# Kernel tuning notes

Measured on AMD Instinct MI355X. Metric: run time of the kernel, lower is better.

Reference implementation:

```python
import jax, jax.numpy as jnp
import numpy as np

H = 16   # nheads
WIN = 64 # window_size (= sqrt(n) so the b,h,n//w,n//w,dk view is valid)


def setup_inputs() -> dict:
    key = jax.random.key(0)
    ks = jax.random.split(key, 7)
    b, n, d = 4, 4096, 1024
    q = jax.random.normal(ks[0], (b, n, d), dtype=jnp.float32)
    k = jax.random.normal(ks[1], (b, n, d), dtype=jnp.float32)
    v = jax.random.normal(ks[2], (b, n, d), dtype=jnp.float32)
    # nn.Linear(d, d, bias=False) weights, stored torch-style as (out, in)
    Wq = jax.random.normal(ks[3], (d, d), dtype=jnp.float32) * 0.02
    Wk = jax.random.normal(ks[4], (d, d), dtype=jnp.float32) * 0.02
    Wv = jax.random.normal(ks[5], (d, d), dtype=jnp.float32) * 0.02
    Wo = jax.random.normal(ks[6], (d, d), dtype=jnp.float32) * 0.02
    return {"q": q, "k": k, "v": v, "Wq": Wq, "Wk": Wk, "Wv": Wv, "Wo": Wo, "window": 1}


def _attention(q, k, v, Wq, Wk, Wv, Wo, window):
    b, qn, d = q.shape
    n = k.shape[1]
    dk = d // H
    # torch Linear: x @ W.T
    qh = (q @ Wq.T).reshape(b, qn, H, dk).transpose(0, 2, 1, 3)  # (b,h,qn,dk)
    kh = (k @ Wk.T).reshape(b, n, H, dk).transpose(0, 2, 1, 3)
    vh = (v @ Wv.T).reshape(b, n, H, dk).transpose(0, 2, 1, 3)
    if window and WIN > 0:
        nw = n // WIN  # requires n == nw*nw, as in the torch .view
        qh = qh.reshape(b, H, nw, nw, dk)
        kh = kh.reshape(b, H, nw, nw, dk)
        vh = vh.reshape(b, H, nw, nw, dk)
    scale = jnp.float32(1.0) / jnp.sqrt(jnp.float32(dk))
    attn = jnp.einsum('...qd,...kd->...qk', qh, kh) * scale  # block-local scores
    attn = jax.nn.softmax(attn, axis=-1)
    o = jnp.einsum('...qk,...kd->...qd', attn, vh)
    # torch: attn.transpose(1, -2).contiguous().view(b, qn, d)
    o = jnp.swapaxes(o, 1, -2).reshape(b, qn, d)
    return o @ Wo.T


def reference(q, k, v, Wq, Wk, Wv, Wo, window):
    return _attention(q, k, v, Wq, Wk, Wv, Wo, window)
```

## Files before the change

kernel.cpp:

```cpp
#include <hip/hip_runtime.h>


typedef unsigned short u16;
typedef unsigned int u32;
typedef __bf16 bf16x8 __attribute__((ext_vector_type(8)));
typedef float f32x4 __attribute__((ext_vector_type(4)));
typedef u16 u16x8 __attribute__((ext_vector_type(8)));

__device__ __forceinline__ u16 f2bf(float f) {
  u32 u = __builtin_bit_cast(u32, f);
  u += 0x7fffu + ((u >> 16) & 1u);
  return (u16)(u >> 16);
}

__device__ __forceinline__ void cvt8_store(const float* __restrict__ src,
                                           u16* __restrict__ dst, size_t i) {
  const float4 a = *(const float4*)(src + i);
  const float4 b = *(const float4*)(src + i + 4);
  u16x8 r;
  r[0] = f2bf(a.x); r[1] = f2bf(a.y); r[2] = f2bf(a.z); r[3] = f2bf(a.w);
  r[4] = f2bf(b.x); r[5] = f2bf(b.y); r[6] = f2bf(b.z); r[7] = f2bf(b.w);
  *(u16x8*)(dst + i) = r;
}

__global__ __launch_bounds__(256) void cvt_kernel(const float* __restrict__ src,
                                                  u16* __restrict__ dst) {
  cvt8_store(src, dst, ((size_t)blockIdx.x * 256 + threadIdx.x) * 8);
}

__global__ __launch_bounds__(256) void cvtw_kernel(
    const float* __restrict__ Wq, const float* __restrict__ Wk,
    const float* __restrict__ Wv, const float* __restrict__ Wo,
    u16* __restrict__ dst) {
  const float* src = (blockIdx.z == 0) ? Wq : (blockIdx.z == 1) ? Wk
                   : (blockIdx.z == 2) ? Wv : Wo;
  cvt8_store(src, dst + (size_t)blockIdx.z * 1048576,
             ((size_t)blockIdx.x * 256 + threadIdx.x) * 8);
}

__device__ __forceinline__ void cp16(const u16* g, u16* l) {
  __builtin_amdgcn_global_load_lds((const __attribute__((address_space(1))) void*)g,
                                   (__attribute__((address_space(3))) void*)l, 16, 0, 0);
}

__global__ __launch_bounds__(256, 2) void gemm_bt_kernel(
    const u16* __restrict__ A, const u16* __restrict__ B, void* __restrict__ Cv,
    int cf) {
  constexpr int N = 1024, K = 1024;
  __shared__ u16 lA[128 * 32];
  __shared__ u16 lB[128 * 32];
  const int tid = threadIdx.x;
  const int lane = tid & 63, w = tid >> 6;
  const int quad = lane >> 4, lr = lane & 15;
  const int lid = blockIdx.x;
  const int xcd = lid & 7, slot = lid >> 3;
  const int m0 = (xcd * 16 + (slot >> 3)) * 128;
  const int n0 = (slot & 7) * 128;
  const int wr = (w >> 1) * 64, wc = (w & 1) * 64;

  const int ch1 = tid, ch2 = tid + 256;
  const u16* Ag1 = A + (size_t)(m0 + (ch1 >> 2)) * K + (ch1 & 3) * 8;
  const u16* Ag2 = A + (size_t)(m0 + (ch2 >> 2)) * K + (ch2 & 3) * 8;
  const u16* Bg1 = B + (size_t)(n0 + (ch1 >> 2)) * K + (ch1 & 3) * 8;
  const u16* Bg2 = B + (size_t)(n0 + (ch2 >> 2)) * K + (ch2 & 3) * 8;

  f32x4 acc[4][4] = {};
  for (int k0 = 0; k0 < K; k0 += 32) {
    cp16(Ag1 + k0, &lA[ch1 * 8]);
    cp16(Ag2 + k0, &lA[ch2 * 8]);
    cp16(Bg1 + k0, &lB[ch1 * 8]);
    cp16(Bg2 + k0, &lB[ch2 * 8]);
    __syncthreads();
    bf16x8 afr[4], bfr[4];
#pragma unroll
    for (int mi = 0; mi < 4; ++mi)
      afr[mi] = *(const bf16x8*)&lA[(wr + mi * 16 + lr) * 32 + quad * 8];
#pragma unroll
    for (int ni = 0; ni < 4; ++ni)
      bfr[ni] = *(const bf16x8*)&lB[(wc + ni * 16 + lr) * 32 + quad * 8];
#pragma unroll
    for (int mi = 0; mi < 4; ++mi)
#pragma unroll
      for (int ni = 0; ni < 4; ++ni)
        acc[mi][ni] = __builtin_amdgcn_mfma_f32_16x16x32_bf16(afr[mi], bfr[ni], acc[mi][ni], 0, 0, 0);
    __syncthreads();
  }
#pragma unroll
  for (int mi = 0; mi < 4; ++mi)
#pragma unroll
    for (int r = 0; r < 4; ++r) {
      const int row = m0 + wr + mi * 16 + quad * 4 + r;
      if (!cf) {
        u16* dst = (u16*)Cv + (size_t)row * N + n0 + wc + lr;
#pragma unroll
        for (int ni = 0; ni < 4; ++ni) dst[ni * 16] = f2bf(acc[mi][ni][r]);
      } else {
        float* dst = (float*)Cv + (size_t)row * N + n0 + wc + lr;
#pragma unroll
        for (int ni = 0; ni < 4; ++ni) dst[ni * 16] = acc[mi][ni][r];
      }
    }
}

__global__ __launch_bounds__(64) void attn_win_kernel(
    const u16* __restrict__ Xq, const u16* __restrict__ Xk, const u16* __restrict__ Xv,
    u16* __restrict__ Xo) {
  __shared__ u16 P[64 * 72];
  const int bx = blockIdx.x;
  const int wi = bx & 63, h = (bx >> 6) & 15, b = bx >> 10;
  const int lane = threadIdx.x & 63, quad = lane >> 4, lr = lane & 15;
  const size_t tb = (size_t)b * 4096 + wi * 64;
  const u16* qb = Xq + tb * 1024 + h * 64;
  const u16* kb = Xk + tb * 1024 + h * 64;
  const u16* vb = Xv + tb * 1024 + h * 64;

  bf16x8 aq[4][2], bk[4][2];
#pragma unroll
  for (int mi = 0; mi < 4; ++mi)
#pragma unroll
    for (int ks = 0; ks < 2; ++ks) {
      aq[mi][ks] = *(const bf16x8*)(qb + (size_t)(mi * 16 + lr) * 1024 + ks * 32 + quad * 8);
      bk[mi][ks] = *(const bf16x8*)(kb + (size_t)(mi * 16 + lr) * 1024 + ks * 32 + quad * 8);
    }
  f32x4 s[4][4];
#pragma unroll
  for (int mi = 0; mi < 4; ++mi)
#pragma unroll
    for (int ni = 0; ni < 4; ++ni) {
      f32x4 z = {0.f, 0.f, 0.f, 0.f};
      z = __builtin_amdgcn_mfma_f32_16x16x32_bf16(aq[mi][0], bk[ni][0], z, 0, 0, 0);
      s[mi][ni] = __builtin_amdgcn_mfma_f32_16x16x32_bf16(aq[mi][1], bk[ni][1], z, 0, 0, 0);
    }

  u16x8 bvr[2][4];
#pragma unroll
  for (int ks = 0; ks < 2; ++ks)
#pragma unroll
    for (int ci = 0; ci < 4; ++ci) {
      const u16* vc = vb + (size_t)(ks * 32 + quad * 8) * 1024 + ci * 16 + lr;
#pragma unroll
      for (int j = 0; j < 8; ++j) bvr[ks][ci][j] = vc[(size_t)j * 1024];
    }

  const float sc = 0.125f;
#pragma unroll
  for (int mi = 0; mi < 4; ++mi)
#pragma unroll
    for (int r = 0; r < 4; ++r) {
      float mx = fmaxf(fmaxf(s[mi][0][r], s[mi][1][r]), fmaxf(s[mi][2][r], s[mi][3][r]));
#pragma unroll
      for (int m = 1; m < 16; m <<= 1) mx = fmaxf(mx, __shfl_xor(mx, m));
      float sum = 0.f;
#pragma unroll
      for (int ni = 0; ni < 4; ++ni) {
        float p = __expf((s[mi][ni][r] - mx) * sc);
        s[mi][ni][r] = p;
        sum += p;
      }
#pragma unroll
      for (int m = 1; m < 16; m <<= 1) sum += __shfl_xor(sum, m);
      const float inv = 1.f / sum;
#pragma unroll
      for (int ni = 0; ni < 4; ++ni) s[mi][ni][r] *= inv;
    }

#pragma unroll
  for (int mi = 0; mi < 4; ++mi)
#pragma unroll
    for (int ni = 0; ni < 4; ++ni)
#pragma unroll
      for (int r = 0; r < 4; ++r)
        P[(mi * 16 + quad * 4 + r) * 72 + ni * 16 + lr] = f2bf(s[mi][ni][r]);
  __syncthreads();

  f32x4 o[4][4] = {};
#pragma unroll
  for (int ks = 0; ks < 2; ++ks) {
    bf16x8 ap[4];
#pragma unroll
    for (int mi = 0; mi < 4; ++mi)
      ap[mi] = *(const bf16x8*)&P[(mi * 16 + lr) * 72 + ks * 32 + quad * 8];
#pragma unroll
    for (int mi = 0; mi < 4; ++mi)
#pragma unroll
      for (int ci = 0; ci < 4; ++ci)
        o[mi][ci] = __builtin_amdgcn_mfma_f32_16x16x32_bf16(
            ap[mi], __builtin_bit_cast(bf16x8, bvr[ks][ci]), o[mi][ci], 0, 0, 0);
  }

#pragma unroll
  for (int mi = 0; mi < 4; ++mi)
#pragma unroll
    for (int r = 0; r < 4; ++r) {
      const int qp = mi * 16 + quad * 4 + r;
      u16* dst = Xo + ((size_t)b * 4096 + (size_t)qp * 64 + wi) * 1024 + h * 64 + lr;
#pragma unroll
      for (int ci = 0; ci < 4; ++ci) dst[ci * 16] = f2bf(o[mi][ci][r]);
    }
}

extern "C" void kernel_launch(void* const* d_in, const int* in_sizes, int n_in,
                              void* d_out, int out_size, void* d_ws, size_t ws_size,
                              hipStream_t stream) {
  (void)in_sizes; (void)n_in; (void)out_size; (void)ws_size;
  const float* q  = (const float*)d_in[0];
  const float* k  = (const float*)d_in[1];
  const float* v  = (const float*)d_in[2];
  const float* Wq = (const float*)d_in[3];
  const float* Wk = (const float*)d_in[4];
  const float* Wv = (const float*)d_in[5];
  const float* Wo = (const float*)d_in[6];

  constexpr size_t ELEMS = (size_t)16384 * 1024;
  u16* Xq = (u16*)d_out;
  u16* qb = (u16*)d_out + ELEMS;
  u16* Wb = (u16*)d_in[0];
  u16* S1 = (u16*)d_ws;
  u16* Xk = S1 + ELEMS;
  u16* Xv = Xk + ELEMS;
  u16* Xo = S1;

  cvt_kernel<<<8192, 256, 0, stream>>>(q, qb);
  cvtw_kernel<<<dim3(512, 1, 4), 256, 0, stream>>>(Wq, Wk, Wv, Wo, Wb);
  cvt_kernel<<<8192, 256, 0, stream>>>(k, S1);
  gemm_bt_kernel<<<1024, 256, 0, stream>>>(qb, Wb, Xq, 0);
  gemm_bt_kernel<<<1024, 256, 0, stream>>>(S1, Wb + 1048576, Xk, 0);
  cvt_kernel<<<8192, 256, 0, stream>>>(v, S1);
  gemm_bt_kernel<<<1024, 256, 0, stream>>>(S1, Wb + 2097152, Xv, 0);
  attn_win_kernel<<<dim3(4096), 64, 0, stream>>>(Xq, Xk, Xv, Xo);
  gemm_bt_kernel<<<1024, 256, 0, stream>>>(Xo, Wb + 3145728, (float*)d_out, 1);
}
```

Measured before the change: 425.3 us.

## Replace GEMM with 256x256-tile, 8-wave, double-buffered LDS-swizzled pipelined kernel

Replaces the 128x128 single-buffer GEMM with a 256x256-tile, 512-thread kernel. It double-buffers LDS across 64-wide K tiles, XOR-swizzles the LDS layout to avoid bank conflicts, and interleaves async global-to-LDS loads with MFMA phases using explicit waitcnt, barriers and setprio. The goal is to hide load latency and raise arithmetic intensity per block. The cost is only 256 blocks for 256 CUs, which means a single wave of work with no tail balancing, plus hand-tuned waitcnt counts that could be fragile.

```diff
diff --git a/kernel.cpp b/kernel.cpp
--- a/kernel.cpp
+++ b/kernel.cpp
@@ -43,59 +43,122 @@
                                    (__attribute__((address_space(3))) void*)l, 16, 0, 0);
 }
 
-__global__ __launch_bounds__(256, 2) void gemm_bt_kernel(
+#define BAR __builtin_amdgcn_s_barrier()
+#define LGKM0                                            \
+  do {                                                   \
+    asm volatile("s_waitcnt lgkmcnt(0)" ::: "memory");   \
+    __builtin_amdgcn_sched_barrier(0);                   \
+  } while (0)
+#define VMC(N) asm volatile("s_waitcnt vmcnt(" #N ")" ::: "memory")
+
+#define MFMA16(MB, KS)                                                       \
+  _Pragma("unroll") for (int m_ = 0; m_ < 4; ++m_)                           \
+  _Pragma("unroll") for (int n_ = 0; n_ < 4; ++n_)                           \
+      acc[(MB) + m_][n_] = __builtin_amdgcn_mfma_f32_16x16x32_bf16(          \
+          af[m_], bfr[KS][n_], acc[(MB) + m_][n_], 0, 0, 0)
+
+#define KTILE(CUR, NXT, KO, ST)                                               \
+  {                                                                           \
+                                    \
+    _Pragma("unroll") for (int m_ = 0; m_ < 4; ++m_)                          \
+        af[m_] = *(const bf16x8*)&LA[CUR][0][abase + m_ * 512];               \
+    _Pragma("unroll") for (int n_ = 0; n_ < 4; ++n_)                          \
+        bfr[0][n_] = *(const bf16x8*)&LB[CUR][0][bbase + n_ * 512];           \
+    if (ST) {                                                                 \
+      cp16(As0 + (KO), &LA[NXT][0][ld0]);                                     \
+      cp16(As0 + 131072 + (KO), &LA[NXT][0][ld0 + 4096]);                     \
+    }                                                                         \
+    BAR; LGKM0;                                                               \
+    __builtin_amdgcn_s_setprio(1); MFMA16(0, 0); __builtin_amdgcn_s_setprio(0);\
+    BAR;                                                                      \
+                                    \
+    _Pragma("unroll") for (int m_ = 0; m_ < 4; ++m_)                          \
+        af[m_] = *(const bf16x8*)&LA[CUR][0][abase + 2048 + m_ * 512];        \
+    if (ST) {                                                                 \
+      cp16(Bs0 + (KO), &LB[NXT][0][ld0]);                                     \
+      cp16(Bs0 + 131072 + (KO), &LB[NXT][0][ld0 + 4096]);                     \
+    }                                                                         \
+    BAR; LGKM0;                                                               \
+    __builtin_amdgcn_s_setprio(1); MFMA16(4, 0); __builtin_amdgcn_s_setprio(0);\
+    if (ST) { VMC(4); } else { VMC(0); }                                      \
+    BAR;                                                                      \
+                                    \
+    _Pragma("unroll") for (int m_ = 0; m_ < 4; ++m_)                          \
+        af[m_] = *(const bf16x8*)&LA[CUR][1][abase + m_ * 512];               \
+    _Pragma("unroll") for (int n_ = 0; n_ < 4; ++n_)                          \
+        bfr[1][n_] = *(const bf16x8*)&LB[CUR][1][bbase + n_ * 512];           \
+    if (ST) {                                                                 \
+      cp16(As0 + 32 + (KO), &LA[NXT][1][ld0]);                                \
+      cp16(As0 + 131104 + (KO), &LA[NXT][1][ld0 + 4096]);                     \
+    }                                                                         \
+    BAR; LGKM0;                                                               \
+    __builtin_amdgcn_s_setprio(1); MFMA16(0, 1); __builtin_amdgcn_s_setprio(0);\
+    BAR;                                                                      \
+                                    \
+    _Pragma("unroll") for (int m_ = 0; m_ < 4; ++m_)                          \
+        af[m_] = *(const bf16x8*)&LA[CUR][1][abase + 2048 + m_ * 512];        \
+    if (ST) {                                                                 \
+      cp16(Bs0 + 32 + (KO), &LB[NXT][1][ld0]);                                \
+      cp16(Bs0 + 131104 + (KO), &LB[NXT][1][ld0 + 4096]);                     \
+    }                                                                         \
+    BAR; LGKM0;                                                               \
+    __builtin_amdgcn_s_setprio(1); MFMA16(4, 1); __builtin_amdgcn_s_setprio(0);\
+    if (ST) { VMC(4); } else { VMC(0); }                                      \
+    BAR;                                                                      \
+  }
+
+__global__ __launch_bounds__(512, 2) void gemm8_kernel(
     const u16* __restrict__ A, const u16* __restrict__ B, void* __restrict__ Cv,
     int cf) {
-  constexpr int N = 1024, K = 1024;
-  __shared__ u16 lA[128 * 32];
-  __shared__ u16 lB[128 * 32];
+  __shared__ u16 LA[2][2][8192];
+  __shared__ u16 LB[2][2][8192];
   const int tid = threadIdx.x;
   const int lane = tid & 63, w = tid >> 6;
+  const int wm = w >> 2, wn = w & 3;
   const int quad = lane >> 4, lr = lane & 15;
-  const int lid = blockIdx.x;
-  const int xcd = lid & 7, slot = lid >> 3;
-  const int m0 = (xcd * 16 + (slot >> 3)) * 128;
-  const int n0 = (slot & 7) * 128;
-  const int wr = (w >> 1) * 64, wc = (w & 1) * 64;
-
-  const int ch1 = tid, ch2 = tid + 256;
-  const u16* Ag1 = A + (size_t)(m0 + (ch1 >> 2)) * K + (ch1 & 3) * 8;
-  const u16* Ag2 = A + (size_t)(m0 + (ch2 >> 2)) * K + (ch2 & 3) * 8;
-  const u16* Bg1 = B + (size_t)(n0 + (ch1 >> 2)) * K + (ch1 & 3) * 8;
-  const u16* Bg2 = B + (size_t)(n0 + (ch2 >> 2)) * K + (ch2 & 3) * 8;
-
-  f32x4 acc[4][4] = {};
-  for (int k0 = 0; k0 < K; k0 += 32) {
-    cp16(Ag1 + k0, &lA[ch1 * 8]);
-    cp16(Ag2 + k0, &lA[ch2 * 8]);
-    cp16(Bg1 + k0, &lB[ch1 * 8]);
-    cp16(Bg2 + k0, &lB[ch2 * 8]);
-    __syncthreads();
-    bf16x8 afr[4], bfr[4];
-#pragma unroll
-    for (int mi = 0; mi < 4; ++mi)
-      afr[mi] = *(const bf16x8*)&lA[(wr + mi * 16 + lr) * 32 + quad * 8];
-#pragma unroll
-    for (int ni = 0; ni < 4; ++ni)
-      bfr[ni] = *(const bf16x8*)&lB[(wc + ni * 16 + lr) * 32 + quad * 8];
-#pragma unroll
-    for (int mi = 0; mi < 4; ++mi)
-#pragma unroll
-      for (int ni = 0; ni < 4; ++ni)
-        acc[mi][ni] = __builtin_amdgcn_mfma_f32_16x16x32_bf16(afr[mi], bfr[ni], acc[mi][ni], 0, 0, 0);
-    __syncthreads();
+  const int swz = (blockIdx.x & 7) * 32 + (blockIdx.x >> 3);
+  const int m0 = (swz & 63) * 256, n0 = (swz >> 6) * 256;
+
+  const int r0 = tid >> 2;
+  const int gsw = ((tid & 3) ^ ((r0 >> 1) & 3)) * 8;
+  const u16* As0 = A + (size_t)(m0 + r0) * 1024 + gsw;
+  const u16* Bs0 = B + (size_t)(n0 + r0) * 1024 + gsw;
+  const int ld0 = tid * 8;
+
+  const int qsw = (quad ^ ((lr >> 1) & 3)) << 3;
+  const int abase = (wm * 128 + lr) * 32 + qsw;
+  const int bbase = (wn * 64 + lr) * 32 + qsw;
+
+  f32x4 acc[8][4] = {};
+  bf16x8 af[4], bfr[2][4];
+
+  cp16(As0, &LA[0][0][ld0]);      cp16(As0 + 131072, &LA[0][0][ld0 + 4096]);
+  cp16(Bs0, &LB[0][0][ld0]);      cp16(Bs0 + 131072, &LB[0][0][ld0 + 4096]);
+  cp16(As0 + 32, &LA[0][1][ld0]); cp16(As0 + 131104, &LA[0][1][ld0 + 4096]);
+  cp16(Bs0 + 32, &LB[0][1][ld0]); cp16(Bs0 + 131104, &LB[0][1][ld0 + 4096]);
+  VMC(4);
+  BAR;
+
+#pragma unroll 1
+  for (int kt = 0; kt < 14; kt += 2) {
+    const int ko1 = (kt + 1) * 64, ko2 = (kt + 2) * 64;
+    KTILE(0, 1, ko1, 1);
+    KTILE(1, 0, ko2, 1);
   }
-#pragma unroll
-  for (int mi = 0; mi < 4; ++mi)
+  KTILE(0, 1, 15 * 64, 1);
+  KTILE(1, 0, 0, 0);
+
+#pragma unroll
+  for (int mi = 0; mi < 8; ++mi)
 #pragma unroll
     for (int r = 0; r < 4; ++r) {
-      const int row = m0 + wr + mi * 16 + quad * 4 + r;
+      const int row = m0 + wm * 128 + mi * 16 + quad * 4 + r;
       if (!cf) {
-        u16* dst = (u16*)Cv + (size_t)row * N + n0 + wc + lr;
+        u16* dst = (u16*)Cv + (size_t)row * 1024 + n0 + wn * 64 + lr;
 #pragma unroll
         for (int ni = 0; ni < 4; ++ni) dst[ni * 16] = f2bf(acc[mi][ni][r]);
       } else {
-        float* dst = (float*)Cv + (size_t)row * N + n0 + wc + lr;
+        float* dst = (float*)Cv + (size_t)row * 1024 + n0 + wn * 64 + lr;
 #pragma unroll
         for (int ni = 0; ni < 4; ++ni) dst[ni * 16] = acc[mi][ni][r];
       }
@@ -223,10 +286,10 @@
   cvt_kernel<<<8192, 256, 0, stream>>>(q, qb);
   cvtw_kernel<<<dim3(512, 1, 4), 256, 0, stream>>>(Wq, Wk, Wv, Wo, Wb);
   cvt_kernel<<<8192, 256, 0, stream>>>(k, S1);
-  gemm_bt_kernel<<<1024, 256, 0, stream>>>(qb, Wb, Xq, 0);
-  gemm_bt_kernel<<<1024, 256, 0, stream>>>(S1, Wb + 1048576, Xk, 0);
+  gemm8_kernel<<<256, 512, 0, stream>>>(qb, Wb, Xq, 0);
+  gemm8_kernel<<<256, 512, 0, stream>>>(S1, Wb + 1048576, Xk, 0);
   cvt_kernel<<<8192, 256, 0, stream>>>(v, S1);
-  gemm_bt_kernel<<<1024, 256, 0, stream>>>(S1, Wb + 2097152, Xv, 0);
+  gemm8_kernel<<<256, 512, 0, stream>>>(S1, Wb + 2097152, Xv, 0);
   attn_win_kernel<<<dim3(4096), 64, 0, stream>>>(Xq, Xk, Xv, Xo);
-  gemm_bt_kernel<<<1024, 256, 0, stream>>>(Xo, Wb + 3145728, (float*)d_out, 1);
-}
+  gemm8_kernel<<<256, 512, 0, stream>>>(Xo, Wb + 3145728, (float*)d_out, 1);
+}
```

New measurement: 420.2 us. About the same (-1.2%).

## Fuse fp32-to-bf16 input conversion into double-buffered GEMM loads

Applied to the files above, without the earlier changes.

Removes the standalone conversion kernels for q, k, v and Wo. The GEMM now reads fp32 tiles directly, converts them to bf16 in registers and writes them into a double-buffered LDS tile, so the next tile's load overlaps the current MFMA step. This drops a full fp32 read plus bf16 write and reread of the activations. In exchange the GEMM reads twice as many bytes of A per tile, uses more registers for the staged float4 values, and converts each row of W many times over.

```diff
diff --git a/kernel.cpp b/kernel.cpp
--- a/kernel.cpp
+++ b/kernel.cpp
@@ -13,29 +13,21 @@
   return (u16)(u >> 16);
 }
 
-__device__ __forceinline__ void cvt8_store(const float* __restrict__ src,
-                                           u16* __restrict__ dst, size_t i) {
-  const float4 a = *(const float4*)(src + i);
-  const float4 b = *(const float4*)(src + i + 4);
+__device__ __forceinline__ u16x8 cvt2(float4 a, float4 b) {
   u16x8 r;
   r[0] = f2bf(a.x); r[1] = f2bf(a.y); r[2] = f2bf(a.z); r[3] = f2bf(a.w);
   r[4] = f2bf(b.x); r[5] = f2bf(b.y); r[6] = f2bf(b.z); r[7] = f2bf(b.w);
-  *(u16x8*)(dst + i) = r;
-}
-
-__global__ __launch_bounds__(256) void cvt_kernel(const float* __restrict__ src,
-                                                  u16* __restrict__ dst) {
-  cvt8_store(src, dst, ((size_t)blockIdx.x * 256 + threadIdx.x) * 8);
-}
-
-__global__ __launch_bounds__(256) void cvtw_kernel(
+  return r;
+}
+
+__global__ __launch_bounds__(256) void cvtw3_kernel(
     const float* __restrict__ Wq, const float* __restrict__ Wk,
-    const float* __restrict__ Wv, const float* __restrict__ Wo,
-    u16* __restrict__ dst) {
-  const float* src = (blockIdx.z == 0) ? Wq : (blockIdx.z == 1) ? Wk
-                   : (blockIdx.z == 2) ? Wv : Wo;
-  cvt8_store(src, dst + (size_t)blockIdx.z * 1048576,
-             ((size_t)blockIdx.x * 256 + threadIdx.x) * 8);
+    const float* __restrict__ Wv, u16* __restrict__ dst) {
+  const float* src = (blockIdx.z == 0) ? Wq : (blockIdx.z == 1) ? Wk : Wv;
+  const size_t i = ((size_t)blockIdx.x * 256 + threadIdx.x) * 8;
+  const float4 a = *(const float4*)(src + i);
+  const float4 b = *(const float4*)(src + i + 4);
+  *(u16x8*)(dst + (size_t)blockIdx.z * 1048576 + i) = cvt2(a, b);
 }
 
 __device__ __forceinline__ void cp16(const u16* g, u16* l) {
@@ -43,12 +35,13 @@
                                    (__attribute__((address_space(3))) void*)l, 16, 0, 0);
 }
 
-__global__ __launch_bounds__(256, 2) void gemm_bt_kernel(
-    const u16* __restrict__ A, const u16* __restrict__ B, void* __restrict__ Cv,
-    int cf) {
+template <int AF32, int BF32, int CF32>
+__global__ __launch_bounds__(256, 2) void gemm_t_kernel(
+    const void* __restrict__ Av, const void* __restrict__ Bv,
+    void* __restrict__ Cv) {
   constexpr int N = 1024, K = 1024;
-  __shared__ u16 lA[128 * 32];
-  __shared__ u16 lB[128 * 32];
+  __shared__ u16 lA[2][128 * 32];
+  __shared__ u16 lB[2][128 * 32];
   const int tid = threadIdx.x;
   const int lane = tid & 63, w = tid >> 6;
   const int quad = lane >> 4, lr = lane & 15;
@@ -59,38 +52,97 @@
   const int wr = (w >> 1) * 64, wc = (w & 1) * 64;
 
   const int ch1 = tid, ch2 = tid + 256;
-  const u16* Ag1 = A + (size_t)(m0 + (ch1 >> 2)) * K + (ch1 & 3) * 8;
-  const u16* Ag2 = A + (size_t)(m0 + (ch2 >> 2)) * K + (ch2 & 3) * 8;
-  const u16* Bg1 = B + (size_t)(n0 + (ch1 >> 2)) * K + (ch1 & 3) * 8;
-  const u16* Bg2 = B + (size_t)(n0 + (ch2 >> 2)) * K + (ch2 & 3) * 8;
+
+  const u16* A16 = (const u16*)Av;
+  const float* A32 = (const float*)Av;
+  const u16* B16 = (const u16*)Bv;
+  const float* B32 = (const float*)Bv;
+
+  const u16* Ag1 = A16 + (size_t)(m0 + (ch1 >> 2)) * K + (ch1 & 3) * 8;
+  const u16* Ag2 = A16 + (size_t)(m0 + (ch2 >> 2)) * K + (ch2 & 3) * 8;
+  const u16* Bg1 = B16 + (size_t)(n0 + (ch1 >> 2)) * K + (ch1 & 3) * 8;
+  const u16* Bg2 = B16 + (size_t)(n0 + (ch2 >> 2)) * K + (ch2 & 3) * 8;
+  const float* Af1 = A32 + (size_t)(m0 + (ch1 >> 2)) * K + (ch1 & 3) * 8;
+  const float* Af2 = A32 + (size_t)(m0 + (ch2 >> 2)) * K + (ch2 & 3) * 8;
+  const float* Bf1 = B32 + (size_t)(n0 + (ch1 >> 2)) * K + (ch1 & 3) * 8;
+  const float* Bf2 = B32 + (size_t)(n0 + (ch2 >> 2)) * K + (ch2 & 3) * 8;
+
+  float4 fA0, fA1, fA2, fA3, fB0, fB1, fB2, fB3;
+
+  if constexpr (AF32) {
+    fA0 = *(const float4*)(Af1);     fA1 = *(const float4*)(Af1 + 4);
+    fA2 = *(const float4*)(Af2);     fA3 = *(const float4*)(Af2 + 4);
+    *(u16x8*)&lA[0][ch1 * 8] = cvt2(fA0, fA1);
+    *(u16x8*)&lA[0][ch2 * 8] = cvt2(fA2, fA3);
+  } else {
+    cp16(Ag1, &lA[0][ch1 * 8]);
+    cp16(Ag2, &lA[0][ch2 * 8]);
+  }
+  if constexpr (BF32) {
+    fB0 = *(const float4*)(Bf1);     fB1 = *(const float4*)(Bf1 + 4);
+    fB2 = *(const float4*)(Bf2);     fB3 = *(const float4*)(Bf2 + 4);
+    *(u16x8*)&lB[0][ch1 * 8] = cvt2(fB0, fB1);
+    *(u16x8*)&lB[0][ch2 * 8] = cvt2(fB2, fB3);
+  } else {
+    cp16(Bg1, &lB[0][ch1 * 8]);
+    cp16(Bg2, &lB[0][ch2 * 8]);
+  }
+  __syncthreads();
 
   f32x4 acc[4][4] = {};
-  for (int k0 = 0; k0 < K; k0 += 32) {
-    cp16(Ag1 + k0, &lA[ch1 * 8]);
-    cp16(Ag2 + k0, &lA[ch2 * 8]);
-    cp16(Bg1 + k0, &lB[ch1 * 8]);
-    cp16(Bg2 + k0, &lB[ch2 * 8]);
+#pragma unroll 1
+  for (int t = 0; t < 32; ++t) {
+    const int cur = t & 1, nxt = cur ^ 1;
+    const int k1 = (t + 1) * 32;
+    const bool more = (t < 31);
+    if (more) {
+      if constexpr (AF32) {
+        fA0 = *(const float4*)(Af1 + k1); fA1 = *(const float4*)(Af1 + k1 + 4);
+        fA2 = *(const float4*)(Af2 + k1); fA3 = *(const float4*)(Af2 + k1 + 4);
+      } else {
+        cp16(Ag1 + k1, &lA[nxt][ch1 * 8]);
+        cp16(Ag2 + k1, &lA[nxt][ch2 * 8]);
+      }
+      if constexpr (BF32) {
+        fB0 = *(const float4*)(Bf1 + k1); fB1 = *(const float4*)(Bf1 + k1 + 4);
+        fB2 = *(const float4*)(Bf2 + k1); fB3 = *(const float4*)(Bf2 + k1 + 4);
+      } else {
+        cp16(Bg1 + k1, &lB[nxt][ch1 * 8]);
+        cp16(Bg2 + k1, &lB[nxt][ch2 * 8]);
+      }
+    }
+    bf16x8 afr[4], bfr[4];
+#pragma unroll
+    for (int mi = 0; mi < 4; ++mi)
+      afr[mi] = *(const bf16x8*)&lA[cur][(wr + mi * 16 + lr) * 32 + quad * 8];
+#pragma unroll
+    for (int ni = 0; ni < 4; ++ni)
+      bfr[ni] = *(const bf16x8*)&lB[cur][(wc + ni * 16 + lr) * 32 + quad * 8];
+#pragma unroll
+    for (int mi = 0; mi < 4; ++mi)
+#pragma unroll
+      for (int ni = 0; ni < 4; ++ni)
+        acc[mi][ni] = __builtin_amdgcn_mfma_f32_16x16x32_bf16(
+            afr[mi], bfr[ni], acc[mi][ni], 0, 0, 0);
+    if (more) {
+      if constexpr (AF32) {
+        *(u16x8*)&lA[nxt][ch1 * 8] = cvt2(fA0, fA1);
+        *(u16x8*)&lA[nxt][ch2 * 8] = cvt2(fA2, fA3);
+      }
+      if constexpr (BF32) {
+        *(u16x8*)&lB[nxt][ch1 * 8] = cvt2(fB0, fB1);
+        *(u16x8*)&lB[nxt][ch2 * 8] = cvt2(fB2, fB3);
+      }
+    }
     __syncthreads();
-    bf16x8 afr[4], bfr[4];
-#pragma unroll
-    for (int mi = 0; mi < 4; ++mi)
-      afr[mi] = *(const bf16x8*)&lA[(wr + mi * 16 + lr) * 32 + quad * 8];
-#pragma unroll
-    for (int ni = 0; ni < 4; ++ni)
-      bfr[ni] = *(const bf16x8*)&lB[(wc + ni * 16 + lr) * 32 + quad * 8];
-#pragma unroll
-    for (int mi = 0; mi < 4; ++mi)
-#pragma unroll
-      for (int ni = 0; ni < 4; ++ni)
-        acc[mi][ni] = __builtin_amdgcn_mfma_f32_16x16x32_bf16(afr[mi], bfr[ni], acc[mi][ni], 0, 0, 0);
-    __syncthreads();
-  }
+  }
+
 #pragma unroll
   for (int mi = 0; mi < 4; ++mi)
 #pragma unroll
     for (int r = 0; r < 4; ++r) {
       const int row = m0 + wr + mi * 16 + quad * 4 + r;
-      if (!cf) {
+      if constexpr (!CF32) {
         u16* dst = (u16*)Cv + (size_t)row * N + n0 + wc + lr;
 #pragma unroll
         for (int ni = 0; ni < 4; ++ni) dst[ni * 16] = f2bf(acc[mi][ni][r]);
@@ -212,21 +264,16 @@
   const float* Wo = (const float*)d_in[6];
 
   constexpr size_t ELEMS = (size_t)16384 * 1024;
-  u16* Xq = (u16*)d_out;
-  u16* qb = (u16*)d_out + ELEMS;
-  u16* Wb = (u16*)d_in[0];
-  u16* S1 = (u16*)d_ws;
-  u16* Xk = S1 + ELEMS;
-  u16* Xv = Xk + ELEMS;
-  u16* Xo = S1;
-
-  cvt_kernel<<<8192, 256, 0, stream>>>(q, qb);
-  cvtw_kernel<<<dim3(512, 1, 4), 256, 0, stream>>>(Wq, Wk, Wv, Wo, Wb);
-  cvt_kernel<<<8192, 256, 0, stream>>>(k, S1);
-  gemm_bt_kernel<<<1024, 256, 0, stream>>>(qb, Wb, Xq, 0);
-  gemm_bt_kernel<<<1024, 256, 0, stream>>>(S1, Wb + 1048576, Xk, 0);
-  cvt_kernel<<<8192, 256, 0, stream>>>(v, S1);
-  gemm_bt_kernel<<<1024, 256, 0, stream>>>(S1, Wb + 2097152, Xv, 0);
+  u16* Xq  = (u16*)d_out;
+  u16* Wb3 = (u16*)d_out + ELEMS;
+  u16* Xo  = (u16*)d_ws;
+  u16* Xk  = Xo + ELEMS;
+  u16* Xv  = Xk + ELEMS;
+
+  cvtw3_kernel<<<dim3(512, 1, 3), 256, 0, stream>>>(Wq, Wk, Wv, Wb3);
+  gemm_t_kernel<1, 0, 0><<<1024, 256, 0, stream>>>(q, Wb3,           Xq);
+  gemm_t_kernel<1, 0, 0><<<1024, 256, 0, stream>>>(k, Wb3 + 1048576, Xk);
+  gemm_t_kernel<1, 0, 0><<<1024, 256, 0, stream>>>(v, Wb3 + 2097152, Xv);
   attn_win_kernel<<<dim3(4096), 64, 0, stream>>>(Xq, Xk, Xv, Xo);
-  gemm_bt_kernel<<<1024, 256, 0, stream>>>(Xo, Wb + 3145728, (float*)d_out, 1);
-}
+  gemm_t_kernel<0, 1, 1><<<1024, 256, 0, stream>>>(Xo, Wo, (float*)d_out);
+}
```

After: 489.0 us. 1.15x slower.
